# Kernel tuning notes

Measured on AMD Instinct MI355X. Metric: run time of the kernel, lower is better.

The kernel has to match this reference:

```python
import jax, jax.numpy as jnp
import numpy as np
from jax import lax

WINS = [3, 5, 7, 11, 15, 19]
MAXW = 19
PAD = MAXW // 2 + 1          # 10, matches F.pad(..., max_wh//2+1)
NEG_HALF = (-MAXW) // 2      # -10, matches torch's `-self.max_wh // 2` (floor div)
EPS_IN = 1e-5
EPS_DEV = 1e-6


def _conv(x, w, b, dil):
    # x: [B,C,H,W], w: [O,I,kh,kw], 'same' padding with dilation
    y = lax.conv_general_dilated(x, w, (1, 1), 'SAME',
                                 rhs_dilation=(dil, dil),
                                 dimension_numbers=('NCHW', 'OIHW', 'NCHW'))
    return y + b[None, :, None, None]


def _inorm_relu(y):
    # InstanceNorm2d(affine=False): per-sample per-channel over H,W, biased var
    m = jnp.mean(y, axis=(2, 3), keepdims=True)
    v = jnp.mean((y - m) ** 2, axis=(2, 3), keepdims=True)
    return jax.nn.relu((y - m) * lax.rsqrt(v + EPS_IN))


def _integral(x):
    # x: [B,H,W,C] -> padded double cumsum (integral image) [B,H+2P,W+2P,C]
    xp = jnp.pad(x, ((0, 0), (PAD, PAD), (PAD, PAD), (0, 0)))
    return jnp.cumsum(jnp.cumsum(xp, axis=1), axis=2)


def _box_sum(ii, h, w):
    # 4-corner integral-image lookup; slices reproduce torch offsets exactly
    top = MAXW // 2 - h // 2
    bot = top + h
    left = MAXW // 2 - w // 2
    right = left + w
    top0 = NEG_HALF - h // 2 - 1
    bot0 = top0 + h
    left0 = NEG_HALF - w // 2 - 1
    right0 = left0 + w
    return (ii[:, top:top0, left:left0] + ii[:, bot:bot0, right:right0]
            - ii[:, top:top0, right:right0] - ii[:, bot:bot0, left:left0])


def _multi_window_mean(x):
    # x: [B,H,W,1] -> [B,n_wins,H,W,1] of window means
    ii = _integral(x)
    cnt_ii = _integral(jnp.ones_like(x[:1]))  # [1,...] pixel-count integral
    means = [_box_sum(ii, hw, hw) / _box_sum(cnt_ii, hw, hw) for hw in WINS]
    return jnp.stack(means, axis=1)


def _sauvola(x1, k, R):
    E_x = _multi_window_mean(x1)
    E_x2 = _multi_window_mean(x1 * x1)
    dev = jnp.sqrt(jnp.maximum(E_x2 - E_x ** 2, EPS_DEV))
    return E_x * (1.0 + k * (dev / R - 1.0))  # [B,n,H,W,1]


def setup_inputs() -> dict:
    key = jax.random.key(0)
    ks = jax.random.split(key, 16)
    B, H, W = 4, 768, 768
    base = 4
    chans = [1, 4, 8, 12, 16, 20, 24]
    d = {'x': jax.random.uniform(ks[0], (B, 1, H, W), dtype=jnp.float32)}
    names = ['conv1', 'convs1', 'convs2', 'convs3', 'convs4', 'convs5']
    for i, nm in enumerate(names):
        cin, cout = chans[i], chans[i + 1]
        d[nm + '_w'] = jax.random.normal(ks[1 + i], (cout, cin, 3, 3), dtype=jnp.float32) * 0.1
        d[nm + '_b'] = jax.random.normal(ks[7 + i], (cout,), dtype=jnp.float32) * 0.01
    d['conv2_w'] = jax.random.normal(ks[13], (len(WINS), 24, 3, 3), dtype=jnp.float32) * 0.1
    d['conv2_b'] = jax.random.normal(ks[14], (len(WINS),), dtype=jnp.float32) * 0.01
    d['k'] = jnp.full((1, len(WINS), 1, 1, 1), 0.2, dtype=jnp.float32)
    d['R'] = jnp.full((1, len(WINS), 1, 1, 1), 0.5, dtype=jnp.float32)
    d['alpha'] = jnp.full((1, 1, 1, 1), 16.0, dtype=jnp.float32)
    return d


def reference(x, conv1_w, conv1_b, convs1_w, convs1_b, convs2_w, convs2_b,
              convs3_w, convs3_b, convs4_w, convs4_b, convs5_w, convs5_b,
              conv2_w, conv2_b, k, R, alpha):
    y = _inorm_relu(_conv(x, conv1_w, conv1_b, 1))
    for w, b in ((convs1_w, convs1_b), (convs2_w, convs2_b), (convs3_w, convs3_b),
                 (convs4_w, convs4_b), (convs5_w, convs5_b)):
        y = _inorm_relu(_conv(y, w, b, 2))
    f = jax.nn.softmax(_conv(y, conv2_w, conv2_b, 1), axis=1)  # [B,n,H,W]
    x1 = jnp.transpose(x, (0, 2, 3, 1))                        # [B,H,W,1]
    th = _sauvola(x1, k, R)                                    # [B,n,H,W,1]
    th1 = jnp.sum(f[..., None] * th, axis=1)                   # [B,H,W,1]
    diff = (x1 - th1) * alpha / (1.0 - 0.0)                    # img_range (0,1)
    return jnp.transpose(diff, (0, 3, 1, 2))                   # [B,1,H,W]
```

## Files before the change

### kernel.cpp

```cpp
#include <hip/hip_runtime.h>
#include <math.h>

#define BDIM 256
typedef __bf16 bf16;
typedef __bf16 bf16x4 __attribute__((ext_vector_type(4)));
typedef __bf16 bf16x8 __attribute__((ext_vector_type(8)));
typedef float f32x4 __attribute__((ext_vector_type(4)));

constexpr int B_ = 4, H_ = 768, W_ = 768;
constexpr int HW_ = H_ * W_;
constexpr int TS = 16;
constexpr int NTB = W_ / TS;
constexpr int NBLK = HW_ / (TS * TS);
constexpr int IH = H_ + 1, IW = W_ + 1;

constexpr size_t SA_BYTES = (size_t)HW_ * 20 * 2;

constexpr int PMAX_FLOATS = 4 * NBLK * 48;
constexpr int OUT_ELEMS   = B_ * HW_;

__device__ void repack_one(const float* __restrict__ src, bf16* __restrict__ dst,
                           int CIN, int CINP, int COUT, int NT16, int KPP)
{
    const int n_ = NT16 * KPP;
    for (int idx = threadIdx.x; idx < n_; idx += BDIM) {
        const int n = idx / KPP, k = idx - n * KPP;
        const int tap = k / CINP, ci = k - tap * CINP;
        float v = 0.f;
        if (n < COUT && tap < 9 && ci < CIN)
            v = src[(n * CIN + ci) * 9 + tap];
        dst[idx] = (bf16)v;
    }
}

__global__ __launch_bounds__(BDIM) void repack_all(
    const float* w0, const float* w1, const float* w2, const float* w3,
    const float* w4, const float* w5, const float* wf,
    bf16* r0, bf16* r1, bf16* r2, bf16* r3, bf16* r4, bf16* r5, bf16* rf)
{
    switch (blockIdx.x) {
        case 0: repack_one(w0, r0, 1,  8,  4,  16, 104); break;
        case 1: repack_one(w1, r1, 4,  8,  8,  16, 104); break;
        case 2: repack_one(w2, r2, 8,  8,  12, 16, 104); break;
        case 3: repack_one(w3, r3, 12, 16, 16, 16, 168); break;
        case 4: repack_one(w4, r4, 16, 16, 20, 32, 168); break;
        case 5: repack_one(w5, r5, 20, 24, 24, 32, 232); break;
        case 6: repack_one(wf, rf, 24, 24, 6,  16, 232); break;
    }
}

template <int CIN, int CINP, int COUT, int DIL, bool FIRST>
__global__ __launch_bounds__(BDIM) void conv_mfma(
    const void* __restrict__ inv,
    const float* __restrict__ prevStats,
    const bf16* __restrict__ wp,
    const float* __restrict__ bias,
    bf16* __restrict__ y,
    float* __restrict__ partials)
{
    constexpr int TW = TS + 2 * DIL;
    constexpr int KP = ((9 * CINP + 31) / 32) * 32;
    constexpr int KPP = KP + 8;
    constexpr int NT = (COUT + 15) / 16;
    constexpr int KS = KP / 32;
    constexpr int CSTR = (CINP == 16) ? 24 : CINP;
    __shared__ __align__(16) bf16 tile[TW * TW * CSTR];
    __shared__ float sred[4][2 * COUT];

    const int s = blockIdx.x / NBLK;
    const int blk = blockIdx.x - s * NBLK;
    const int ti = blk / NTB, tj = blk - ti * NTB;
    const int i0 = ti * TS - DIL, j0 = tj * TS - DIL;
    const int t = threadIdx.x;

    for (int loc = t; loc < TW * TW; loc += BDIM) {
        const int rr = loc / TW, cc = loc - rr * TW;
        const int gi = i0 + rr, gj = j0 + cc;
        const bool ok = (gi >= 0) & (gi < H_) & (gj >= 0) & (gj < W_);
        float lv[CSTR];
#pragma unroll
        for (int c = 0; c < CSTR; ++c) lv[c] = 0.f;
        if (ok) {
            if constexpr (FIRST) {
                const float* xg = (const float*)inv + (size_t)s * HW_;
                lv[0] = xg[(size_t)gi * W_ + gj];
            } else {
                const bf16* ing = (const bf16*)inv +
                                  ((size_t)s * HW_ + (size_t)gi * W_ + gj) * CIN;
                const float* ps = prevStats + s * 2 * CIN;
                if constexpr (CIN % 8 == 0) {
#pragma unroll
                    for (int qq = 0; qq < CIN / 8; ++qq) {
                        bf16x8 raw = ((const bf16x8*)ing)[qq];
#pragma unroll
                        for (int u = 0; u < 8; ++u) {
                            const int ci = 8 * qq + u;
                            lv[ci] = fmaxf(((float)raw[u] - ps[2 * ci]) * ps[2 * ci + 1], 0.f);
                        }
                    }
                } else {
#pragma unroll
                    for (int qq = 0; qq < CIN / 4; ++qq) {
                        bf16x4 raw = ((const bf16x4*)ing)[qq];
#pragma unroll
                        for (int u = 0; u < 4; ++u) {
                            const int ci = 4 * qq + u;
                            lv[ci] = fmaxf(((float)raw[u] - ps[2 * ci]) * ps[2 * ci + 1], 0.f);
                        }
                    }
                }
            }
        }
        bf16* lp = tile + loc * CSTR;
#pragma unroll
        for (int g = 0; g < CSTR / 4; ++g) {
            bf16x4 pk = { (bf16)lv[4 * g], (bf16)lv[4 * g + 1],
                          (bf16)lv[4 * g + 2], (bf16)lv[4 * g + 3] };
            *(bf16x4*)(lp + 4 * g) = pk;
        }
    }
    __syncthreads();

    const int wave = t >> 6, lane = t & 63, q = lane >> 4, ln = lane & 15;
    f32x4 acc[4][NT];
#pragma unroll
    for (int mt = 0; mt < 4; ++mt)
#pragma unroll
        for (int u = 0; u < NT; ++u) acc[mt][u] = (f32x4){0.f, 0.f, 0.f, 0.f};

    auto aOff = [&](int ks) -> int {
        int k0 = ks * 32 + q * 8;
        int tap = k0 / CINP;
        int ci0 = k0 - tap * CINP;
        if (tap > 8) { tap = 0; ci0 = 0; }
        const int ky = tap / 3, kx = tap - 3 * ky;
        return (ky * DIL * TW + kx * DIL) * CSTR + ci0;
    };

    bf16x8 bfr[NT], bfrN[NT];
    bf16x8 af[4], afN[4];
#pragma unroll
    for (int u = 0; u < NT; ++u)
        bfr[u] = *(const bf16x8*)&wp[(u * 16 + ln) * KPP + q * 8];
    {
        const int ao = aOff(0);
#pragma unroll
        for (int mt = 0; mt < 4; ++mt)
            af[mt] = *(const bf16x8*)&tile[((wave * 4 + mt) * TW + ln) * CSTR + ao];
    }

#pragma unroll
    for (int ks = 0; ks < KS; ++ks) {
        if (ks + 1 < KS) {
#pragma unroll
            for (int u = 0; u < NT; ++u)
                bfrN[u] = *(const bf16x8*)&wp[(u * 16 + ln) * KPP + (ks + 1) * 32 + q * 8];
            const int ao = aOff(ks + 1);
#pragma unroll
            for (int mt = 0; mt < 4; ++mt)
                afN[mt] = *(const bf16x8*)&tile[((wave * 4 + mt) * TW + ln) * CSTR + ao];
        }
#pragma unroll
        for (int mt = 0; mt < 4; ++mt)
#pragma unroll
            for (int u = 0; u < NT; ++u)
                acc[mt][u] = __builtin_amdgcn_mfma_f32_16x16x32_bf16(
                    af[mt], bfr[u], acc[mt][u], 0, 0, 0);
#pragma unroll
        for (int u = 0; u < NT; ++u) bfr[u] = bfrN[u];
#pragma unroll
        for (int mt = 0; mt < 4; ++mt) af[mt] = afN[mt];
    }

#pragma unroll
    for (int u = 0; u < NT; ++u) {
        const int n = u * 16 + ln;
        const float bv = (n < COUT) ? bias[n] : 0.f;
        float s1 = 0.f, s2 = 0.f;
#pragma unroll
        for (int mt = 0; mt < 4; ++mt)
#pragma unroll
            for (int r = 0; r < 4; ++r) {
                const float v = acc[mt][u][r] + bv;
                acc[mt][u][r] = v;
                s1 += v; s2 += v * v;
            }
        s1 += __shfl_xor(s1, 16); s1 += __shfl_xor(s1, 32);
        s2 += __shfl_xor(s2, 16); s2 += __shfl_xor(s2, 32);
        if (lane < 16 && n < COUT) { sred[wave][n] = s1; sred[wave][COUT + n] = s2; }
    }
    __syncthreads();
    if (t < 2 * COUT) {
        partials[((size_t)s * NBLK + blk) * (2 * COUT) + t] =
            sred[0][t] + sred[1][t] + sred[2][t] + sred[3][t];
    }

    bf16* ost = tile;
#pragma unroll
    for (int u = 0; u < NT; ++u) {
        const int n = u * 16 + ln;
        if (n < COUT) {
#pragma unroll
            for (int mt = 0; mt < 4; ++mt)
#pragma unroll
                for (int r = 0; r < 4; ++r) {
                    const int pl = (wave * 4 + mt) * 16 + q * 4 + r;
                    ost[pl * COUT + n] = (bf16)acc[mt][u][r];
                }
        }
    }
    __syncthreads();

    const int lr = t >> 4, lc = t & 15;
    bf16* yp = y + (size_t)s * HW_ * COUT +
               ((size_t)(ti * TS + lr) * W_ + (tj * TS + lc)) * COUT;
    const bf16* sp = ost + t * COUT;
    if constexpr (COUT % 8 == 0) {
#pragma unroll
        for (int g = 0; g < COUT / 8; ++g)
            ((bf16x8*)yp)[g] = ((const bf16x8*)sp)[g];
    } else {
#pragma unroll
        for (int g = 0; g < COUT / 4; ++g)
            ((bf16x4*)yp)[g] = ((const bf16x4*)sp)[g];
    }
}

template <int COUT>
__global__ __launch_bounds__(BDIM) void reduce_stats(
    const float* __restrict__ partials, float* __restrict__ stats)
{
    const int s = blockIdx.x / COUT;
    const int co = blockIdx.x - s * COUT;
    const float* P = partials + (size_t)s * NBLK * (2 * COUT);
    float s1 = 0.f, s2 = 0.f;
    for (int k = threadIdx.x; k < NBLK; k += BDIM) {
        const float* p = P + (size_t)k * (2 * COUT);
        s1 += p[co];
        s2 += p[COUT + co];
    }
#pragma unroll
    for (int off = 32; off; off >>= 1) {
        s1 += __shfl_xor(s1, off);
        s2 += __shfl_xor(s2, off);
    }
    __shared__ float l1[4], l2[4];
    const int lane = threadIdx.x & 63, wave = threadIdx.x >> 6;
    if (lane == 0) { l1[wave] = s1; l2[wave] = s2; }
    __syncthreads();
    if (threadIdx.x == 0) {
        float t1 = l1[0] + l1[1] + l1[2] + l1[3];
        float t2 = l2[0] + l2[1] + l2[2] + l2[3];
        float m = t1 / (float)HW_;
        float var = t2 / (float)HW_ - m * m;
        stats[((size_t)s * COUT + co) * 2 + 0] = m;
        stats[((size_t)s * COUT + co) * 2 + 1] = rsqrtf(var + 1e-5f);
    }
}

__global__ __launch_bounds__(BDIM) void conv2_softmax_mfma(
    const bf16* __restrict__ in, const float* __restrict__ prevStats,
    const bf16* __restrict__ wp, const float* __restrict__ bias,
    char* __restrict__ wsA)
{
    constexpr int CIN = 24, CINP = 24, COUT = 6, DIL = 1;
    constexpr int TW = TS + 2 * DIL;
    constexpr int KPP = 232, KS = 7, CSTR = 24;
    __shared__ __align__(16) bf16 tile[TW * TW * CSTR];

    const int s = blockIdx.x / NBLK;
    const int blk = blockIdx.x - s * NBLK;
    const int ti = blk / NTB, tj = blk - ti * NTB;
    const int i0 = ti * TS - DIL, j0 = tj * TS - DIL;
    const int t = threadIdx.x;

    const float* ps = prevStats + s * 2 * CIN;
    for (int loc = t; loc < TW * TW; loc += BDIM) {
        const int rr = loc / TW, cc = loc - rr * TW;
        const int gi = i0 + rr, gj = j0 + cc;
        const bool ok = (gi >= 0) & (gi < H_) & (gj >= 0) & (gj < W_);
        float lv[CSTR];
#pragma unroll
        for (int c = 0; c < CSTR; ++c) lv[c] = 0.f;
        if (ok) {
            const bf16* ing = in + ((size_t)s * HW_ + (size_t)gi * W_ + gj) * CIN;
#pragma unroll
            for (int qq = 0; qq < CIN / 8; ++qq) {
                bf16x8 raw = ((const bf16x8*)ing)[qq];
#pragma unroll
                for (int u = 0; u < 8; ++u) {
                    const int ci = 8 * qq + u;
                    lv[ci] = fmaxf(((float)raw[u] - ps[2 * ci]) * ps[2 * ci + 1], 0.f);
                }
            }
        }
        bf16* lp = tile + loc * CSTR;
#pragma unroll
        for (int g = 0; g < CSTR / 4; ++g) {
            bf16x4 pk = { (bf16)lv[4 * g], (bf16)lv[4 * g + 1],
                          (bf16)lv[4 * g + 2], (bf16)lv[4 * g + 3] };
            *(bf16x4*)(lp + 4 * g) = pk;
        }
    }
    __syncthreads();

    const int wave = t >> 6, lane = t & 63, q = lane >> 4, ln = lane & 15;
    f32x4 acc[4];
#pragma unroll
    for (int mt = 0; mt < 4; ++mt) acc[mt] = (f32x4){0.f, 0.f, 0.f, 0.f};

    auto aOff = [&](int ks) -> int {
        int k0 = ks * 32 + q * 8;
        int tap = k0 / CINP;
        int ci0 = k0 - tap * CINP;
        if (tap > 8) { tap = 0; ci0 = 0; }
        const int ky = tap / 3, kx = tap - 3 * ky;
        return (ky * DIL * TW + kx * DIL) * CSTR + ci0;
    };

    bf16x8 bfr, bfrN;
    bf16x8 af[4], afN[4];
    bfr = *(const bf16x8*)&wp[ln * KPP + q * 8];
    {
        const int ao = aOff(0);
#pragma unroll
        for (int mt = 0; mt < 4; ++mt)
            af[mt] = *(const bf16x8*)&tile[((wave * 4 + mt) * TW + ln) * CSTR + ao];
    }
#pragma unroll
    for (int ks = 0; ks < KS; ++ks) {
        if (ks + 1 < KS) {
            bfrN = *(const bf16x8*)&wp[ln * KPP + (ks + 1) * 32 + q * 8];
            const int ao = aOff(ks + 1);
#pragma unroll
            for (int mt = 0; mt < 4; ++mt)
                afN[mt] = *(const bf16x8*)&tile[((wave * 4 + mt) * TW + ln) * CSTR + ao];
        }
#pragma unroll
        for (int mt = 0; mt < 4; ++mt)
            acc[mt] = __builtin_amdgcn_mfma_f32_16x16x32_bf16(af[mt], bfr, acc[mt], 0, 0, 0);
        bfr = bfrN;
#pragma unroll
        for (int mt = 0; mt < 4; ++mt) af[mt] = afN[mt];
    }

    __syncthreads();
    float* slog = (float*)tile;
    const float bv = (ln < COUT) ? bias[ln] : 0.f;
#pragma unroll
    for (int mt = 0; mt < 4; ++mt)
#pragma unroll
        for (int r = 0; r < 4; ++r)
            if (ln < COUT) {
                const int pl = (wave * 4 + mt) * 16 + q * 4 + r;
                slog[pl * COUT + ln] = acc[mt][r] + bv;
            }
    __syncthreads();

    float e[COUT];
    float mx = slog[t * COUT];
#pragma unroll
    for (int co = 1; co < COUT; ++co) mx = fmaxf(mx, slog[t * COUT + co]);
    float sm = 0.f;
#pragma unroll
    for (int co = 0; co < COUT; ++co) { e[co] = __expf(slog[t * COUT + co] - mx); sm += e[co]; }
    const float inv = 1.f / sm;
    bf16* f = (bf16*)(wsA + (size_t)s * SA_BYTES);
    const int prow = ti * TS + (t >> 4), pcol = tj * TS + (t & 15);
    bf16* fp = f + ((size_t)prow * W_ + pcol) * 6;
#pragma unroll
    for (int co = 0; co < COUT; ++co) fp[co] = (bf16)(e[co] * inv);
}

__global__ __launch_bounds__(BDIM) void sauvola_fused(
    const float* __restrict__ x, const char* __restrict__ wsA,
    const float* __restrict__ kArr, const float* __restrict__ RArr,
    const float* __restrict__ alphaP, float* __restrict__ outp)
{
    constexpr int R9 = 9;
    constexpr int TSW = TS + 2 * R9;
    constexpr int PSTR = 36;
    __shared__ float I1[35 * PSTR];
    __shared__ float I2[35 * PSTR];

    const int s = blockIdx.x / NBLK;
    const int blk = blockIdx.x - s * NBLK;
    const int ti = blk / NTB, tj = blk - ti * NTB;
    const int i0 = ti * TS - R9, j0 = tj * TS - R9;
    const int t = threadIdx.x;
    const float* xs = x + (size_t)s * HW_;

    for (int loc = t; loc < TSW * TSW; loc += BDIM) {
        const int rr = loc / TSW, cc = loc - rr * TSW;
        const int gi = i0 + rr, gj = j0 + cc;
        float v = 0.f;
        if ((gi >= 0) & (gi < H_) & (gj >= 0) & (gj < W_))
            v = xs[(size_t)gi * W_ + gj];
        I1[(rr + 1) * PSTR + cc + 1] = v;
        I2[(rr + 1) * PSTR + cc + 1] = v * v;
    }
    for (int idx = t; idx < 2 * (35 + 34); idx += BDIM) {
        const int arr = idx / (35 + 34);
        const int r2 = idx - arr * (35 + 34);
        float* P = arr ? I2 : I1;
        if (r2 < 35) P[r2] = 0.f;
        else P[(r2 - 35 + 1) * PSTR] = 0.f;
    }
    __syncthreads();

    if (t < 68) {
        float* P = (t >= 34) ? I2 : I1;
        float* row = P + ((t >= 34 ? t - 34 : t) + 1) * PSTR;
        float a = 0.f;
#pragma unroll 2
        for (int c = 1; c <= TSW; ++c) { a += row[c]; row[c] = a; }
    }
    __syncthreads();

    if (t < 68) {
        float* P = (t >= 34) ? I2 : I1;
        const int c = (t >= 34 ? t - 34 : t) + 1;
        float a = 0.f;
#pragma unroll 2
        for (int r = 1; r <= TSW; ++r) { a += P[r * PSTR + c]; P[r * PSTR + c] = a; }
    }
    __syncthreads();

    const int lr = t >> 4, lc = t & 15;
    const int gi = ti * TS + lr, gj = tj * TS + lc;
    const float xv = xs[(size_t)gi * W_ + gj];
    const bf16* fp = (const bf16*)(wsA + (size_t)s * SA_BYTES) +
                     ((size_t)gi * W_ + gj) * 6;
    const float alpha = alphaP[0];

    const int wins[6] = {3, 5, 7, 11, 15, 19};
    float th1 = 0.f;
#pragma unroll
    for (int wi = 0; wi < 6; ++wi) {
        const int r = wins[wi] >> 1;
        const int r0 = max(gi - r, 0), r1i = min(gi + r, H_ - 1);
        const int c0 = max(gj - r, 0), c1 = min(gj + r, W_ - 1);
        const float invc = 1.f / (float)((r1i - r0 + 1) * (c1 - c0 + 1));
        const int top = lr + R9 - r, bot = lr + R9 + r + 1;
        const int lef = lc + R9 - r, rig = lc + R9 + r + 1;
        const float s1 = I1[bot * PSTR + rig] - I1[top * PSTR + rig]
                       - I1[bot * PSTR + lef] + I1[top * PSTR + lef];
        const float s2 = I2[bot * PSTR + rig] - I2[top * PSTR + rig]
                       - I2[bot * PSTR + lef] + I2[top * PSTR + lef];
        const float Ex = s1 * invc;
        const float Ex2 = s2 * invc;
        const float dev = sqrtf(fmaxf(Ex2 - Ex * Ex, 1e-6f));
        const float th = Ex * (1.f + kArr[wi] * (dev / RArr[wi] - 1.f));
        th1 = fmaf((float)fp[wi], th, th1);
    }
    outp[(size_t)s * HW_ + (size_t)gi * W_ + gj] = (xv - th1) * alpha;
}

extern "C" void kernel_launch(void* const* d_in, const int* in_sizes, int n_in,
                              void* d_out, int out_size, void* d_ws, size_t ws_size,
                              hipStream_t stream) {
    const float* x   = (const float*)d_in[0];
    const float* w0  = (const float*)d_in[1];  const float* b0 = (const float*)d_in[2];
    const float* w1  = (const float*)d_in[3];  const float* b1 = (const float*)d_in[4];
    const float* w2  = (const float*)d_in[5];  const float* b2 = (const float*)d_in[6];
    const float* w3  = (const float*)d_in[7];  const float* b3 = (const float*)d_in[8];
    const float* w4  = (const float*)d_in[9];  const float* b4 = (const float*)d_in[10];
    const float* w5  = (const float*)d_in[11]; const float* b5 = (const float*)d_in[12];
    const float* wf  = (const float*)d_in[13]; const float* bf = (const float*)d_in[14];
    const float* kA  = (const float*)d_in[15];
    const float* RA  = (const float*)d_in[16];
    const float* alp = (const float*)d_in[17];
    float* out = (float*)d_out;
    (void)n_in; (void)in_sizes; (void)out_size;

    float* partials = out + (OUT_ELEMS - PMAX_FLOATS - 256);
    float* stats    = out + (OUT_ELEMS - 224);

    auto need = [](int nb) -> size_t {
        size_t o = 0;
        auto al = [&](size_t bytes) { o += (bytes + 255) & ~(size_t)255; };
        al((size_t)nb * HW_ * 20 * 2);
        al((size_t)nb * HW_ * 24 * 2);
        al(1664 * 2); al(1664 * 2); al(1664 * 2); al(2688 * 2);
        al(5376 * 2); al(7424 * 2); al(3712 * 2);
        return o;
    };
    int nb = 1;
    if (ws_size >= need(4)) nb = 4;
    else if (ws_size >= need(2)) nb = 2;

    char* ws = (char*)d_ws;
    size_t off = 0;
    auto alloc = [&](size_t bytes) -> void* {
        void* p = ws + off;
        off += (bytes + 255) & ~(size_t)255;
        return p;
    };
    bf16*  bufA = (bf16*)alloc((size_t)nb * HW_ * 20 * 2);
    bf16*  bufB = (bf16*)alloc((size_t)nb * HW_ * 24 * 2);
    bf16* r0 = (bf16*)alloc(1664 * 2);
    bf16* r1 = (bf16*)alloc(1664 * 2);
    bf16* r2 = (bf16*)alloc(1664 * 2);
    bf16* r3 = (bf16*)alloc(2688 * 2);
    bf16* r4 = (bf16*)alloc(5376 * 2);
    bf16* r5 = (bf16*)alloc(7424 * 2);
    bf16* rf = (bf16*)alloc(3712 * 2);
    char* wsA = (char*)bufA;

    const dim3 blk(BDIM);
    const int cg = nb * NBLK;

    repack_all<<<7, blk, 0, stream>>>(w0, w1, w2, w3, w4, w5, wf,
                                      r0, r1, r2, r3, r4, r5, rf);

    for (int it = 0; it < B_ / nb; ++it) {
        const float* xc   = x   + (size_t)it * nb * HW_;
        float*       outc = out + (size_t)it * nb * HW_;

        conv_mfma<1, 8, 4, 1, true><<<cg, blk, 0, stream>>>(xc, nullptr, r0, b0, bufA, partials);
        reduce_stats<4><<<nb * 4, blk, 0, stream>>>(partials, stats);

        conv_mfma<4, 8, 8, 2, false><<<cg, blk, 0, stream>>>(bufA, stats, r1, b1, bufB, partials);
        reduce_stats<8><<<nb * 8, blk, 0, stream>>>(partials, stats);

        conv_mfma<8, 8, 12, 2, false><<<cg, blk, 0, stream>>>(bufB, stats, r2, b2, bufA, partials);
        reduce_stats<12><<<nb * 12, blk, 0, stream>>>(partials, stats);

        conv_mfma<12, 16, 16, 2, false><<<cg, blk, 0, stream>>>(bufA, stats, r3, b3, bufB, partials);
        reduce_stats<16><<<nb * 16, blk, 0, stream>>>(partials, stats);

        conv_mfma<16, 16, 20, 2, false><<<cg, blk, 0, stream>>>(bufB, stats, r4, b4, bufA, partials);
        reduce_stats<20><<<nb * 20, blk, 0, stream>>>(partials, stats);

        conv_mfma<20, 24, 24, 2, false><<<cg, blk, 0, stream>>>(bufA, stats, r5, b5, bufB, partials);
        reduce_stats<24><<<nb * 24, blk, 0, stream>>>(partials, stats);

        conv2_softmax_mfma<<<cg, blk, 0, stream>>>(bufB, stats, rf, bf, wsA);

        sauvola_fused<<<cg, blk, 0, stream>>>(xc, wsA, kA, RA, alp, outc);
    }
}
```

Baseline: 416.7 us.

## Fuse final conv+softmax with Sauvola thresholding into one kernel

Merges the conv2/softmax kernel with the Sauvola kernel so softmax weights stay in registers instead of being written to and read back from a global workspace. The integral-image staging is interleaved with the conv tile load and MFMA phase. This removes one launch and the intermediate global traffic, at the cost of more shared memory per block and a longer kernel.

```diff
diff --git a/kernel.cpp b/kernel.cpp
--- a/kernel.cpp
+++ b/kernel.cpp
@@ -12,9 +12,6 @@
 constexpr int TS = 16;
 constexpr int NTB = W_ / TS;
 constexpr int NBLK = HW_ / (TS * TS);
-constexpr int IH = H_ + 1, IW = W_ + 1;
-
-constexpr size_t SA_BYTES = (size_t)HW_ * 20 * 2;
 
 constexpr int PMAX_FLOATS = 4 * NBLK * 48;
 constexpr int OUT_ELEMS   = B_ * HW_;
@@ -258,21 +255,30 @@
     }
 }
 
-__global__ __launch_bounds__(BDIM) void conv2_softmax_mfma(
+__global__ __launch_bounds__(BDIM) void conv2_sauvola(
     const bf16* __restrict__ in, const float* __restrict__ prevStats,
     const bf16* __restrict__ wp, const float* __restrict__ bias,
-    char* __restrict__ wsA)
+    const float* __restrict__ x,
+    const float* __restrict__ kArr, const float* __restrict__ RArr,
+    const float* __restrict__ alphaP, float* __restrict__ outp)
 {
     constexpr int CIN = 24, CINP = 24, COUT = 6, DIL = 1;
     constexpr int TW = TS + 2 * DIL;
     constexpr int KPP = 232, KS = 7, CSTR = 24;
+    constexpr int R9 = 9;
+    constexpr int TSW = TS + 2 * R9;
+    constexpr int PSTR = 36;
     __shared__ __align__(16) bf16 tile[TW * TW * CSTR];
+    __shared__ float I1[35 * PSTR];
+    __shared__ float I2[35 * PSTR];
 
     const int s = blockIdx.x / NBLK;
     const int blk = blockIdx.x - s * NBLK;
     const int ti = blk / NTB, tj = blk - ti * NTB;
     const int i0 = ti * TS - DIL, j0 = tj * TS - DIL;
+    const int is0 = ti * TS - R9, js0 = tj * TS - R9;
     const int t = threadIdx.x;
+    const float* xs = x + (size_t)s * HW_;
 
     const float* ps = prevStats + s * 2 * CIN;
     for (int loc = t; loc < TW * TW; loc += BDIM) {
@@ -301,6 +307,22 @@
                           (bf16)lv[4 * g + 2], (bf16)lv[4 * g + 3] };
             *(bf16x4*)(lp + 4 * g) = pk;
         }
+    }
+    for (int loc = t; loc < TSW * TSW; loc += BDIM) {
+        const int rr = loc / TSW, cc = loc - rr * TSW;
+        const int gi = is0 + rr, gj = js0 + cc;
+        float v = 0.f;
+        if ((gi >= 0) & (gi < H_) & (gj >= 0) & (gj < W_))
+            v = xs[(size_t)gi * W_ + gj];
+        I1[(rr + 1) * PSTR + cc + 1] = v;
+        I2[(rr + 1) * PSTR + cc + 1] = v * v;
+    }
+    for (int idx = t; idx < 2 * (35 + 34); idx += BDIM) {
+        const int arr = idx / (35 + 34);
+        const int r2 = idx - arr * (35 + 34);
+        float* P = arr ? I2 : I1;
+        if (r2 < 35) P[r2] = 0.f;
+        else P[(r2 - 35 + 1) * PSTR] = 0.f;
     }
     __syncthreads();
 
@@ -343,8 +365,8 @@
 #pragma unroll
         for (int mt = 0; mt < 4; ++mt) af[mt] = afN[mt];
     }
-
-    __syncthreads();
+    __syncthreads();
+
     float* slog = (float*)tile;
     const float bv = (ln < COUT) ? bias[ln] : 0.f;
 #pragma unroll
@@ -355,59 +377,6 @@
                 const int pl = (wave * 4 + mt) * 16 + q * 4 + r;
                 slog[pl * COUT + ln] = acc[mt][r] + bv;
             }
-    __syncthreads();
-
-    float e[COUT];
-    float mx = slog[t * COUT];
-#pragma unroll
-    for (int co = 1; co < COUT; ++co) mx = fmaxf(mx, slog[t * COUT + co]);
-    float sm = 0.f;
-#pragma unroll
-    for (int co = 0; co < COUT; ++co) { e[co] = __expf(slog[t * COUT + co] - mx); sm += e[co]; }
-    const float inv = 1.f / sm;
-    bf16* f = (bf16*)(wsA + (size_t)s * SA_BYTES);
-    const int prow = ti * TS + (t >> 4), pcol = tj * TS + (t & 15);
-    bf16* fp = f + ((size_t)prow * W_ + pcol) * 6;
-#pragma unroll
-    for (int co = 0; co < COUT; ++co) fp[co] = (bf16)(e[co] * inv);
-}
-
-__global__ __launch_bounds__(BDIM) void sauvola_fused(
-    const float* __restrict__ x, const char* __restrict__ wsA,
-    const float* __restrict__ kArr, const float* __restrict__ RArr,
-    const float* __restrict__ alphaP, float* __restrict__ outp)
-{
-    constexpr int R9 = 9;
-    constexpr int TSW = TS + 2 * R9;
-    constexpr int PSTR = 36;
-    __shared__ float I1[35 * PSTR];
-    __shared__ float I2[35 * PSTR];
-
-    const int s = blockIdx.x / NBLK;
-    const int blk = blockIdx.x - s * NBLK;
-    const int ti = blk / NTB, tj = blk - ti * NTB;
-    const int i0 = ti * TS - R9, j0 = tj * TS - R9;
-    const int t = threadIdx.x;
-    const float* xs = x + (size_t)s * HW_;
-
-    for (int loc = t; loc < TSW * TSW; loc += BDIM) {
-        const int rr = loc / TSW, cc = loc - rr * TSW;
-        const int gi = i0 + rr, gj = j0 + cc;
-        float v = 0.f;
-        if ((gi >= 0) & (gi < H_) & (gj >= 0) & (gj < W_))
-            v = xs[(size_t)gi * W_ + gj];
-        I1[(rr + 1) * PSTR + cc + 1] = v;
-        I2[(rr + 1) * PSTR + cc + 1] = v * v;
-    }
-    for (int idx = t; idx < 2 * (35 + 34); idx += BDIM) {
-        const int arr = idx / (35 + 34);
-        const int r2 = idx - arr * (35 + 34);
-        float* P = arr ? I2 : I1;
-        if (r2 < 35) P[r2] = 0.f;
-        else P[(r2 - 35 + 1) * PSTR] = 0.f;
-    }
-    __syncthreads();
-
     if (t < 68) {
         float* P = (t >= 34) ? I2 : I1;
         float* row = P + ((t >= 34 ? t - 34 : t) + 1) * PSTR;
@@ -424,13 +393,23 @@
 #pragma unroll 2
         for (int r = 1; r <= TSW; ++r) { a += P[r * PSTR + c]; P[r * PSTR + c] = a; }
     }
+    float e[COUT];
+    {
+        float mx = slog[t * COUT];
+#pragma unroll
+        for (int co = 1; co < COUT; ++co) mx = fmaxf(mx, slog[t * COUT + co]);
+        float sm = 0.f;
+#pragma unroll
+        for (int co = 0; co < COUT; ++co) { e[co] = __expf(slog[t * COUT + co] - mx); sm += e[co]; }
+        const float inv = 1.f / sm;
+#pragma unroll
+        for (int co = 0; co < COUT; ++co) e[co] *= inv;
+    }
     __syncthreads();
 
     const int lr = t >> 4, lc = t & 15;
     const int gi = ti * TS + lr, gj = tj * TS + lc;
     const float xv = xs[(size_t)gi * W_ + gj];
-    const bf16* fp = (const bf16*)(wsA + (size_t)s * SA_BYTES) +
-                     ((size_t)gi * W_ + gj) * 6;
     const float alpha = alphaP[0];
 
     const int wins[6] = {3, 5, 7, 11, 15, 19};
@@ -451,7 +430,7 @@
         const float Ex2 = s2 * invc;
         const float dev = sqrtf(fmaxf(Ex2 - Ex * Ex, 1e-6f));
         const float th = Ex * (1.f + kArr[wi] * (dev / RArr[wi] - 1.f));
-        th1 = fmaf((float)fp[wi], th, th1);
+        th1 = fmaf(e[wi], th, th1);
     }
     outp[(size_t)s * HW_ + (size_t)gi * W_ + gj] = (xv - th1) * alpha;
 }
@@ -505,7 +484,6 @@
     bf16* r4 = (bf16*)alloc(5376 * 2);
     bf16* r5 = (bf16*)alloc(7424 * 2);
     bf16* rf = (bf16*)alloc(3712 * 2);
-    char* wsA = (char*)bufA;
 
     const dim3 blk(BDIM);
     const int cg = nb * NBLK;
@@ -535,8 +513,7 @@
         conv_mfma<20, 24, 24, 2, false><<<cg, blk, 0, stream>>>(bufA, stats, r5, b5, bufB, partials);
         reduce_stats<24><<<nb * 24, blk, 0, stream>>>(partials, stats);
 
-        conv2_softmax_mfma<<<cg, blk, 0, stream>>>(bufB, stats, rf, bf, wsA);
-
-        sauvola_fused<<<cg, blk, 0, stream>>>(xc, wsA, kA, RA, alp, outc);
+        conv2_sauvola<<<cg, blk, 0, stream>>>(
+            bufB, stats, rf, bf, xc, kA, RA, alp, outc);
     }
 }
```

New measurement: 416.0 us. No clear change (-0.2%).
